# Kernel optimization log

Measured on AMD Instinct MI355X. Metric: run time of the kernel, lower is better.

Reference implementation:

```python
import jax, jax.numpy as jnp
import numpy as np

N = 100000      # nodes
E = 1600000     # edges (avg degree 16)
D_IN = 128
D_OUT = 128
P = 0.5         # dropout prob (module is in training mode)


def setup_inputs() -> dict:
    key = jax.random.key(0)
    k1, k2, k3 = jax.random.split(key, 3)
    x = jax.random.normal(k1, (N, D_IN), dtype=jnp.float32)
    edge_index = jax.random.randint(k2, (2, E), 0, N, dtype=jnp.int32)
    # GCNConv learned params (glorot-ish weight, zero bias)
    weight = jax.random.normal(k3, (D_IN, D_OUT), dtype=jnp.float32) / np.float32(np.sqrt(D_IN))
    bias = jnp.zeros((D_OUT,), dtype=jnp.float32)
    return {"x": x, "edge_index": edge_index, "weight": weight, "bias": bias}


def reference(x, edge_index, weight, bias):
    # --- GCNConv: add self-loops, symmetric deg^-1/2 normalization ---
    loops = jnp.arange(N, dtype=edge_index.dtype)
    src = jnp.concatenate([edge_index[0], loops])   # [E+N]
    dst = jnp.concatenate([edge_index[1], loops])   # [E+N]
    deg = jax.ops.segment_sum(jnp.ones_like(dst, dtype=x.dtype), dst, num_segments=N)
    dinv = jnp.where(deg > 0, jax.lax.rsqrt(deg), 0.0)          # deg^-1/2
    norm = dinv[src] * dinv[dst]                                # [E+N]
    h = x @ weight                                              # [N, D_OUT]
    msgs = h[src] * norm[:, None]                               # gather + scale
    out = jax.ops.segment_sum(msgs, dst, num_segments=N) + bias # scatter-add
    # --- ReLU ---
    out = jax.nn.relu(out)
    # --- Dropout (training=True), fixed key for determinism ---
    keep = jax.random.bernoulli(jax.random.key(42), 1.0 - P, out.shape)
    return jnp.where(keep, out / (1.0 - P), jnp.zeros((), out.dtype))
```

## Files before the change

kernel.cpp:

```cpp
#include <hip/hip_runtime.h>

#define N_NODES 100000
#define E_EDGES 1600000
#define D 128
#define PAD 136
#define GEMM_BLKS 1563
#define SCHUNK 4096
#define SCAT_BLKS ((E_EDGES + SCHUNK - 1) / SCHUNK)
#define RANGE 98
#define NR 1024
#define RCAP 2048
#define CAP 2048
#define NPW 13

typedef __attribute__((ext_vector_type(8))) short short8;
typedef __attribute__((ext_vector_type(8))) unsigned short ushort8v;
typedef __attribute__((ext_vector_type(4))) float f32x4;

__device__ __forceinline__ unsigned int rotl32(unsigned int x, int r) {
  return (x << r) | (x >> (32 - r));
}

__device__ __forceinline__ unsigned int threefry_bits(unsigned int ctr) {
  const unsigned int ks0 = 0u, ks1 = 42u;
  const unsigned int ks2 = ks0 ^ ks1 ^ 0x1BD11BDAu;
  unsigned int x0 = ks0;
  unsigned int x1 = ctr + ks1;
#define TF_ROUND(R) { x0 += x1; x1 = rotl32(x1, R); x1 ^= x0; }
  TF_ROUND(13) TF_ROUND(15) TF_ROUND(26) TF_ROUND(6)
  x0 += ks1; x1 += ks2 + 1u;
  TF_ROUND(17) TF_ROUND(29) TF_ROUND(16) TF_ROUND(24)
  x0 += ks2; x1 += ks0 + 2u;
  TF_ROUND(13) TF_ROUND(15) TF_ROUND(26) TF_ROUND(6)
  x0 += ks0; x1 += ks1 + 3u;
  TF_ROUND(17) TF_ROUND(29) TF_ROUND(16) TF_ROUND(24)
  x0 += ks1; x1 += ks2 + 4u;
  TF_ROUND(13) TF_ROUND(15) TF_ROUND(26) TF_ROUND(6)
  x0 += ks2; x1 += ks0 + 5u;
#undef TF_ROUND
  return x0 ^ x1;
}

__device__ __forceinline__ unsigned short f2bf(float f) {
  unsigned int u = __float_as_uint(f);
  u = (u + 0x7FFFu + ((u >> 16) & 1u)) >> 16;
  return (unsigned short)u;
}
__device__ __forceinline__ float bf2f_lo(unsigned int v) {
  return __uint_as_float(v << 16);
}
__device__ __forceinline__ float bf2f_hi(unsigned int v) {
  return __uint_as_float(v & 0xFFFF0000u);
}

__global__ __launch_bounds__(256) void k_init(const float* __restrict__ w,
                                              unsigned short* __restrict__ wbf,
                                              int* __restrict__ cur) {
  int t = blockIdx.x * 256 + threadIdx.x;
  int k = t >> 7;
  int n = t & 127;
  wbf[n * 128 + k] = f2bf(w[t]);
  if (t < NR) cur[t] = t * RCAP;
}

__global__ __launch_bounds__(256) void k_fused(const float* __restrict__ x,
                                               const unsigned short* __restrict__ wbf,
                                               unsigned short* __restrict__ h,
                                               const int* __restrict__ ei,
                                               int* __restrict__ cur,
                                               int* __restrict__ ebuf) {
  __shared__ unsigned short Wl[128 * PAD];
  __shared__ unsigned short Xl[64 * PAD];
  const int t = threadIdx.x;

  if (blockIdx.x < SCAT_BLKS) {
    int* lcnt = (int*)Xl;
    int* gb   = lcnt + NR;
    int* sc2  = gb + NR;
    const int e0 = blockIdx.x * SCHUNK;
    for (int i = t; i < NR; i += 256) { lcnt[i] = 0; sc2[i] = 0; }
    __syncthreads();
#pragma unroll
    for (int i = 0; i < SCHUNK / 256; ++i) {
      int e = e0 + i * 256 + t;
      if (e < E_EDGES) atomicAdd(&lcnt[ei[E_EDGES + e] / RANGE], 1);
    }
    __syncthreads();
    for (int i = t; i < NR; i += 256) {
      int c = lcnt[i];
      gb[i] = c ? atomicAdd(&cur[i], c) : 0;
    }
    __syncthreads();
#pragma unroll
    for (int i = 0; i < SCHUNK / 256; ++i) {
      int e = e0 + i * 256 + t;
      if (e < E_EDGES) {
        int d = ei[E_EDGES + e];
        int s = ei[e];
        int b = d / RANGE;
        int dl = d - b * RANGE;
        int pos = gb[b] + atomicAdd(&sc2[b], 1);
        if (pos < (b + 1) * RCAP)
          ebuf[pos] = s | (dl << 17);
      }
    }
    return;
  }

  const int row0 = (blockIdx.x - SCAT_BLKS) * 64;

#pragma unroll
  for (int i = 0; i < 8; ++i) {
    int u  = t + i * 256;
    int kg = u & 15;
    int n  = u >> 4;
    *(ushort8v*)&Wl[n * PAD + kg * 8] = *(const ushort8v*)&wbf[n * 128 + kg * 8];
  }
  const float4* x4 = (const float4*)x;
#pragma unroll
  for (int i = 0; i < 8; ++i) {
    int id = t + i * 256;
    int r  = id >> 5;
    int c4 = id & 31;
    int row = row0 + r; if (row >= N_NODES) row = N_NODES - 1;
    float4 v = x4[(long long)row * 32 + c4];
    ushort4 p;
    p.x = f2bf(v.x); p.y = f2bf(v.y); p.z = f2bf(v.z); p.w = f2bf(v.w);
    *(ushort4*)&Xl[r * PAD + c4 * 4] = p;
  }
  __syncthreads();

  const int wv   = t >> 6;
  const int l    = t & 63;
  const int quad = l >> 4;
  const int ln16 = l & 15;
  const int m0   = wv * 16;

  short8 a[4];
#pragma unroll
  for (int kt = 0; kt < 4; ++kt)
    a[kt] = *(const short8*)&Xl[(m0 + ln16) * PAD + kt * 32 + quad * 8];

#pragma unroll
  for (int nt = 0; nt < 8; ++nt) {
    f32x4 acc = {0.f, 0.f, 0.f, 0.f};
#pragma unroll
    for (int kt = 0; kt < 4; ++kt) {
      short8 b = *(const short8*)&Wl[(nt * 16 + ln16) * PAD + kt * 32 + quad * 8];
      acc = __builtin_amdgcn_mfma_f32_16x16x32_bf16(a[kt], b, acc, 0, 0, 0);
    }
#pragma unroll
    for (int r = 0; r < 4; ++r)
      Xl[(m0 + quad * 4 + r) * PAD + nt * 16 + ln16] = f2bf(acc[r]);
  }

#pragma unroll
  for (int v = 0; v < 4; ++v) {
    int idx = v * 64 + l;
    int rr  = idx >> 4;
    int ch  = idx & 15;
    int row = row0 + m0 + rr;
    if (row < N_NODES)
      *(ushort8v*)&h[(long long)row * D + ch * 8] = *(const ushort8v*)&Xl[(m0 + rr) * PAD + ch * 8];
  }
}

__global__ __launch_bounds__(256) void k_deg(const int* __restrict__ ebuf,
                                             const int* __restrict__ cur,
                                             float* __restrict__ dinv) {
  __shared__ int hist[128];
  const int t = threadIdx.x;
  const int r = blockIdx.x;
  if (t < 128) hist[t] = 0;
  __syncthreads();
  const int lo = r * RCAP;
  const int hi = min(cur[r], lo + RCAP);
  for (int e = lo + t; e < hi; e += 256)
    atomicAdd(&hist[((unsigned)ebuf[e]) >> 17], 1);
  __syncthreads();
  if (t < RANGE) {
    int n = r * RANGE + t;
    if (n < N_NODES) dinv[n] = rsqrtf((float)(hist[t] + 1));
  }
}

__global__ __launch_bounds__(512) void k_agg(const int* __restrict__ ebuf,
                                             const int* __restrict__ cur,
                                             const float* __restrict__ dinv,
                                             const unsigned short* __restrict__ h,
                                             const float* __restrict__ bias,
                                             float* __restrict__ out) {
  __shared__ int ssort[CAP];
  __shared__ int shist[128];
  __shared__ int sscn[128];
  __shared__ int scur[128];
  const int t  = threadIdx.x;
  const int r  = blockIdx.x;
  const int wv = t >> 6;
  const int l  = t & 63;
  const unsigned int* h32 = (const unsigned int*)h;

  float a0[NPW], a1[NPW];
#pragma unroll
  for (int j = 0; j < NPW; ++j) { a0[j] = 0.f; a1[j] = 0.f; }

  const int lo = r * RCAP;
  const int hi = min(cur[r], lo + RCAP);

  for (int c0 = lo; c0 < hi; c0 += CAP) {
    const int m = min(CAP, hi - c0);
    if (t < 128) shist[t] = 0;
    __syncthreads();

    int pk0 = -1, pk1 = -1, pk2 = -1, pk3 = -1;
    {
      int i0 = t, i1 = t + 512, i2 = t + 1024, i3 = t + 1536;
      if (i0 < m) { pk0 = ebuf[c0 + i0]; atomicAdd(&shist[((unsigned)pk0) >> 17], 1); }
      if (i1 < m) { pk1 = ebuf[c0 + i1]; atomicAdd(&shist[((unsigned)pk1) >> 17], 1); }
      if (i2 < m) { pk2 = ebuf[c0 + i2]; atomicAdd(&shist[((unsigned)pk2) >> 17], 1); }
      if (i3 < m) { pk3 = ebuf[c0 + i3]; atomicAdd(&shist[((unsigned)pk3) >> 17], 1); }
    }
    __syncthreads();

    if (t < 128) sscn[t] = shist[t];
    __syncthreads();
    for (int off = 1; off < 128; off <<= 1) {
      int xv = (t < 128 && t >= off) ? sscn[t - off] : 0;
      __syncthreads();
      if (t < 128) sscn[t] += xv;
      __syncthreads();
    }
    if (t < 128) scur[t] = sscn[t] - shist[t];
    __syncthreads();

    if (pk0 != -1) ssort[atomicAdd(&scur[((unsigned)pk0) >> 17], 1)] = pk0 & 0x1FFFF;
    if (pk1 != -1) ssort[atomicAdd(&scur[((unsigned)pk1) >> 17], 1)] = pk1 & 0x1FFFF;
    if (pk2 != -1) ssort[atomicAdd(&scur[((unsigned)pk2) >> 17], 1)] = pk2 & 0x1FFFF;
    if (pk3 != -1) ssort[atomicAdd(&scur[((unsigned)pk3) >> 17], 1)] = pk3 & 0x1FFFF;
    __syncthreads();

#pragma unroll
    for (int j = 0; j < NPW; ++j) {
      int nl = wv + 8 * j;
      if (nl < RANGE) {
        int s1i = sscn[nl];
        int s0i = s1i - shist[nl];
        float aa0 = a0[j], aa1 = a1[j];
#pragma unroll 4
        for (int e = s0i; e < s1i; ++e) {
          int s = ssort[e];
          float wgt = dinv[s];
          unsigned u = h32[(long long)s * 64 + l];
          aa0 = fmaf(bf2f_lo(u), wgt, aa0);
          aa1 = fmaf(bf2f_hi(u), wgt, aa1);
        }
        a0[j] = aa0; a1[j] = aa1;
      }
    }
    __syncthreads();
  }

#pragma unroll
  for (int j = 0; j < NPW; ++j) {
    int nl = wv + 8 * j;
    if (nl >= RANGE) continue;
    int n = r * RANGE + nl;
    if (n >= N_NODES) continue;
    float dv = dinv[n];
    unsigned hv = h32[(long long)n * 64 + l];
    float v0 = (a0[j] + bf2f_lo(hv) * dv) * dv;
    float v1 = (a1[j] + bf2f_hi(hv) * dv) * dv;
    float2 bb = ((const float2*)bias)[l];
    float r0 = fmaxf(v0 + bb.x, 0.f);
    float r1 = fmaxf(v1 + bb.y, 0.f);
    unsigned i0 = (unsigned)n * 128u + (unsigned)(2 * l);
    unsigned b0 = threefry_bits(i0);
    unsigned b1 = threefry_bits(i0 + 1u);
    float2 res;
    res.x = (b0 & 0x80000000u) ? 0.0f : r0 * 2.0f;
    res.y = (b1 & 0x80000000u) ? 0.0f : r1 * 2.0f;
    ((float2*)out)[(long long)n * 64 + l] = res;
  }
}

extern "C" void kernel_launch(void* const* d_in, const int* in_sizes, int n_in,
                              void* d_out, int out_size, void* d_ws, size_t ws_size,
                              hipStream_t stream) {
  const float* x    = (const float*)d_in[0];
  const int*   ei   = (const int*)d_in[1];
  const float* w    = (const float*)d_in[2];
  const float* bias = (const float*)d_in[3];
  float* out = (float*)d_out;

  char* p = (char*)d_ws;
  unsigned short* h   = (unsigned short*)p;  p += (size_t)N_NODES * D * 2;
  unsigned short* wbf = (unsigned short*)p;  p += 128 * 128 * 2;
  float* dinv = (float*)p;                   p += (size_t)(NR * RANGE) * 4;
  int* cur    = (int*)p;                     p += NR * 4;
  int* ebuf   = (int*)p;                     p += (size_t)NR * RCAP * 4;

  k_init<<<64, 256, 0, stream>>>(w, wbf, cur);
  k_fused<<<SCAT_BLKS + GEMM_BLKS, 256, 0, stream>>>(x, wbf, h, ei, cur, ebuf);
  k_deg<<<NR, 256, 0, stream>>>(ebuf, cur, dinv);
  k_agg<<<NR, 512, 0, stream>>>(ebuf, cur, dinv, h, bias, out);
}
```

Baseline: 225.4 us.

## Split fused scatter/GEMM kernel and simplify aggregation to a single chunk

```diff
diff --git a/kernel.cpp b/kernel.cpp
--- a/kernel.cpp
+++ b/kernel.cpp
@@ -63,51 +63,74 @@
   if (t < NR) cur[t] = t * RCAP;
 }
 
-__global__ __launch_bounds__(256) void k_fused(const float* __restrict__ x,
-                                               const unsigned short* __restrict__ wbf,
-                                               unsigned short* __restrict__ h,
-                                               const int* __restrict__ ei,
-                                               int* __restrict__ cur,
-                                               int* __restrict__ ebuf) {
+__global__ __launch_bounds__(256) void k_scat(const int* __restrict__ ei,
+                                              int* __restrict__ cur,
+                                              int* __restrict__ ebuf) {
+  __shared__ int lcnt[NR];
+  __shared__ int gb[NR];
+  __shared__ int sc2[NR];
+  const int t = threadIdx.x;
+  const int e0 = blockIdx.x * SCHUNK;
+  for (int i = t; i < NR; i += 256) { lcnt[i] = 0; sc2[i] = 0; }
+  __syncthreads();
+  int myd[SCHUNK / 256];
+#pragma unroll
+  for (int i = 0; i < SCHUNK / 256; ++i) {
+    int e = e0 + i * 256 + t;
+    myd[i] = -1;
+    if (e < E_EDGES) {
+      int d = ei[E_EDGES + e];
+      myd[i] = d;
+      atomicAdd(&lcnt[d / RANGE], 1);
+    }
+  }
+  __syncthreads();
+  for (int i = t; i < NR; i += 256) {
+    int c = lcnt[i];
+    gb[i] = c ? atomicAdd(&cur[i], c) : 0;
+  }
+  __syncthreads();
+#pragma unroll
+  for (int i = 0; i < SCHUNK / 256; ++i) {
+    int d = myd[i];
+    if (d >= 0) {
+      int e = e0 + i * 256 + t;
+      int s = ei[e];
+      int b = d / RANGE;
+      int dl = d - b * RANGE;
+      int pos = gb[b] + atomicAdd(&sc2[b], 1);
+      if (pos < (b + 1) * RCAP)
+        ebuf[pos] = s | (dl << 17);
+    }
+  }
+}
+
+__global__ __launch_bounds__(256) void k_deg(const int* __restrict__ ebuf,
+                                             const int* __restrict__ cur,
+                                             float* __restrict__ dinv) {
+  __shared__ int hist[128];
+  const int t = threadIdx.x;
+  const int r = blockIdx.x;
+  if (t < 128) hist[t] = 0;
+  __syncthreads();
+  const int lo = r * RCAP;
+  const int hi = min(cur[r], lo + RCAP);
+  for (int e = lo + t; e < hi; e += 256)
+    atomicAdd(&hist[((unsigned)ebuf[e]) >> 17], 1);
+  __syncthreads();
+  if (t < RANGE) {
+    int n = r * RANGE + t;
+    if (n < N_NODES) dinv[n] = rsqrtf((float)(hist[t] + 1));
+  }
+}
+
+__global__ __launch_bounds__(256) void k_gemm(const float* __restrict__ x,
+                                              const unsigned short* __restrict__ wbf,
+                                              unsigned short* __restrict__ h) {
   __shared__ unsigned short Wl[128 * PAD];
   __shared__ unsigned short Xl[64 * PAD];
   const int t = threadIdx.x;
-
-  if (blockIdx.x < SCAT_BLKS) {
-    int* lcnt = (int*)Xl;
-    int* gb   = lcnt + NR;
-    int* sc2  = gb + NR;
-    const int e0 = blockIdx.x * SCHUNK;
-    for (int i = t; i < NR; i += 256) { lcnt[i] = 0; sc2[i] = 0; }
-    __syncthreads();
-#pragma unroll
-    for (int i = 0; i < SCHUNK / 256; ++i) {
-      int e = e0 + i * 256 + t;
-      if (e < E_EDGES) atomicAdd(&lcnt[ei[E_EDGES + e] / RANGE], 1);
-    }
-    __syncthreads();
-    for (int i = t; i < NR; i += 256) {
-      int c = lcnt[i];
-      gb[i] = c ? atomicAdd(&cur[i], c) : 0;
-    }
-    __syncthreads();
-#pragma unroll
-    for (int i = 0; i < SCHUNK / 256; ++i) {
-      int e = e0 + i * 256 + t;
-      if (e < E_EDGES) {
-        int d = ei[E_EDGES + e];
-        int s = ei[e];
-        int b = d / RANGE;
-        int dl = d - b * RANGE;
-        int pos = gb[b] + atomicAdd(&sc2[b], 1);
-        if (pos < (b + 1) * RCAP)
-          ebuf[pos] = s | (dl << 17);
-      }
-    }
-    return;
-  }
-
-  const int row0 = (blockIdx.x - SCAT_BLKS) * 64;
+  const int row0 = blockIdx.x * 64;
 
 #pragma unroll
   for (int i = 0; i < 8; ++i) {
@@ -162,25 +185,6 @@
     int row = row0 + m0 + rr;
     if (row < N_NODES)
       *(ushort8v*)&h[(long long)row * D + ch * 8] = *(const ushort8v*)&Xl[(m0 + rr) * PAD + ch * 8];
-  }
-}
-
-__global__ __launch_bounds__(256) void k_deg(const int* __restrict__ ebuf,
-                                             const int* __restrict__ cur,
-                                             float* __restrict__ dinv) {
-  __shared__ int hist[128];
-  const int t = threadIdx.x;
-  const int r = blockIdx.x;
-  if (t < 128) hist[t] = 0;
-  __syncthreads();
-  const int lo = r * RCAP;
-  const int hi = min(cur[r], lo + RCAP);
-  for (int e = lo + t; e < hi; e += 256)
-    atomicAdd(&hist[((unsigned)ebuf[e]) >> 17], 1);
-  __syncthreads();
-  if (t < RANGE) {
-    int n = r * RANGE + t;
-    if (n < N_NODES) dinv[n] = rsqrtf((float)(hist[t] + 1));
   }
 }
 
@@ -205,59 +209,55 @@
   for (int j = 0; j < NPW; ++j) { a0[j] = 0.f; a1[j] = 0.f; }
 
   const int lo = r * RCAP;
-  const int hi = min(cur[r], lo + RCAP);
-
-  for (int c0 = lo; c0 < hi; c0 += CAP) {
-    const int m = min(CAP, hi - c0);
-    if (t < 128) shist[t] = 0;
+  const int m  = min(cur[r], lo + RCAP) - lo;
+
+  if (t < 128) shist[t] = 0;
+  __syncthreads();
+
+  int pk0 = -1, pk1 = -1, pk2 = -1, pk3 = -1;
+  {
+    int i0 = t, i1 = t + 512, i2 = t + 1024, i3 = t + 1536;
+    if (i0 < m) { pk0 = ebuf[lo + i0]; atomicAdd(&shist[((unsigned)pk0) >> 17], 1); }
+    if (i1 < m) { pk1 = ebuf[lo + i1]; atomicAdd(&shist[((unsigned)pk1) >> 17], 1); }
+    if (i2 < m) { pk2 = ebuf[lo + i2]; atomicAdd(&shist[((unsigned)pk2) >> 17], 1); }
+    if (i3 < m) { pk3 = ebuf[lo + i3]; atomicAdd(&shist[((unsigned)pk3) >> 17], 1); }
+  }
+  __syncthreads();
+
+  if (t < 128) sscn[t] = shist[t];
+  __syncthreads();
+  for (int off = 1; off < 128; off <<= 1) {
+    int xv = (t < 128 && t >= off) ? sscn[t - off] : 0;
     __syncthreads();
-
-    int pk0 = -1, pk1 = -1, pk2 = -1, pk3 = -1;
-    {
-      int i0 = t, i1 = t + 512, i2 = t + 1024, i3 = t + 1536;
-      if (i0 < m) { pk0 = ebuf[c0 + i0]; atomicAdd(&shist[((unsigned)pk0) >> 17], 1); }
-      if (i1 < m) { pk1 = ebuf[c0 + i1]; atomicAdd(&shist[((unsigned)pk1) >> 17], 1); }
-      if (i2 < m) { pk2 = ebuf[c0 + i2]; atomicAdd(&shist[((unsigned)pk2) >> 17], 1); }
-      if (i3 < m) { pk3 = ebuf[c0 + i3]; atomicAdd(&shist[((unsigned)pk3) >> 17], 1); }
+    if (t < 128) sscn[t] += xv;
+    __syncthreads();
+  }
+  if (t < 128) scur[t] = sscn[t] - shist[t];
+  __syncthreads();
+
+  if (pk0 != -1) ssort[atomicAdd(&scur[((unsigned)pk0) >> 17], 1)] = pk0 & 0x1FFFF;
+  if (pk1 != -1) ssort[atomicAdd(&scur[((unsigned)pk1) >> 17], 1)] = pk1 & 0x1FFFF;
+  if (pk2 != -1) ssort[atomicAdd(&scur[((unsigned)pk2) >> 17], 1)] = pk2 & 0x1FFFF;
+  if (pk3 != -1) ssort[atomicAdd(&scur[((unsigned)pk3) >> 17], 1)] = pk3 & 0x1FFFF;
+  __syncthreads();
+
+#pragma unroll
+  for (int j = 0; j < NPW; ++j) {
+    int nl = wv + 8 * j;
+    if (nl < RANGE) {
+      int s1i = sscn[nl];
+      int s0i = s1i - shist[nl];
+      float aa0 = a0[j], aa1 = a1[j];
+#pragma unroll 4
+      for (int e = s0i; e < s1i; ++e) {
+        int s = ssort[e];
+        float wgt = dinv[s];
+        unsigned u = h32[(long long)s * 64 + l];
+        aa0 = fmaf(bf2f_lo(u), wgt, aa0);
+        aa1 = fmaf(bf2f_hi(u), wgt, aa1);
+      }
+      a0[j] = aa0; a1[j] = aa1;
     }
-    __syncthreads();
-
-    if (t < 128) sscn[t] = shist[t];
-    __syncthreads();
-    for (int off = 1; off < 128; off <<= 1) {
-      int xv = (t < 128 && t >= off) ? sscn[t - off] : 0;
-      __syncthreads();
-      if (t < 128) sscn[t] += xv;
-      __syncthreads();
-    }
-    if (t < 128) scur[t] = sscn[t] - shist[t];
-    __syncthreads();
-
-    if (pk0 != -1) ssort[atomicAdd(&scur[((unsigned)pk0) >> 17], 1)] = pk0 & 0x1FFFF;
-    if (pk1 != -1) ssort[atomicAdd(&scur[((unsigned)pk1) >> 17], 1)] = pk1 & 0x1FFFF;
-    if (pk2 != -1) ssort[atomicAdd(&scur[((unsigned)pk2) >> 17], 1)] = pk2 & 0x1FFFF;
-    if (pk3 != -1) ssort[atomicAdd(&scur[((unsigned)pk3) >> 17], 1)] = pk3 & 0x1FFFF;
-    __syncthreads();
-
-#pragma unroll
-    for (int j = 0; j < NPW; ++j) {
-      int nl = wv + 8 * j;
-      if (nl < RANGE) {
-        int s1i = sscn[nl];
-        int s0i = s1i - shist[nl];
-        float aa0 = a0[j], aa1 = a1[j];
-#pragma unroll 4
-        for (int e = s0i; e < s1i; ++e) {
-          int s = ssort[e];
-          float wgt = dinv[s];
-          unsigned u = h32[(long long)s * 64 + l];
-          aa0 = fmaf(bf2f_lo(u), wgt, aa0);
-          aa1 = fmaf(bf2f_hi(u), wgt, aa1);
-        }
-        a0[j] = aa0; a1[j] = aa1;
-      }
-    }
-    __syncthreads();
   }
 
 #pragma unroll
@@ -266,7 +266,7 @@
     if (nl >= RANGE) continue;
     int n = r * RANGE + nl;
     if (n >= N_NODES) continue;
-    float dv = dinv[n];
+    float dv = rsqrtf((float)(shist[nl] + 1));
     unsigned hv = h32[(long long)n * 64 + l];
     float v0 = (a0[j] + bf2f_lo(hv) * dv) * dv;
     float v1 = (a1[j] + bf2f_hi(hv) * dv) * dv;
@@ -300,7 +300,8 @@
   int* ebuf   = (int*)p;                     p += (size_t)NR * RCAP * 4;
 
   k_init<<<64, 256, 0, stream>>>(w, wbf, cur);
-  k_fused<<<SCAT_BLKS + GEMM_BLKS, 256, 0, stream>>>(x, wbf, h, ei, cur, ebuf);
+  k_scat<<<SCAT_BLKS, 256, 0, stream>>>(ei, cur, ebuf);
   k_deg<<<NR, 256, 0, stream>>>(ebuf, cur, dinv);
+  k_gemm<<<GEMM_BLKS, 256, 0, stream>>>(x, wbf, h);
   k_agg<<<NR, 512, 0, stream>>>(ebuf, cur, dinv, h, bias, out);
 }
```

Result: no change. 225.0 us (-0.1%).
